# Kernel tuning notes

Measured on AMD Instinct MI355X. Metric: run time of the kernel, lower is better.

## Reference

```python
import jax, jax.numpy as jnp
import numpy as np

NEG_SLOPE = 0.2
EPS = 1e-6


def setup_inputs() -> dict:
    key = jax.random.key(0)
    k1, k2 = jax.random.split(key)
    B, C, N = 4, 64, 32768
    x = jax.random.normal(k1, (B, C, 3, N), dtype=jnp.float32)
    # VNLinear weight: nn.Linear(in, out, bias=False).weight -> [out, in]
    W = jax.random.normal(k2, (C, C), dtype=jnp.float32) * (1.0 / np.sqrt(C))
    return {"x": x, "W": W}


def reference(x, W):
    # VNLinear: kron(W, eye(3)) conv2d == per-3-vector channel mix
    # d[b,o,v,n] = sum_i W[o,i] * x[b,i,v,n]
    d = jnp.einsum('oi,bivn->bovn', W, x)
    dotprod = jnp.sum(x * d, axis=2, keepdims=True)      # [B,C,1,N]
    d_norm_sq = jnp.sum(d * d, axis=2, keepdims=True)    # [B,C,1,N]
    neg = x - (1.0 - NEG_SLOPE) * (dotprod / (d_norm_sq + EPS)) * d
    return jnp.where(dotprod >= 0, x, neg)
```

## Files before the change

kernel.cpp:

```cpp
#include <hip/hip_runtime.h>

#define NEG_SLOPE 0.2f
#define EPS 1e-6f


#define C_CH 64
#define V_DIM 3
#define N_FULL 32768
#define NT 32
#define THREADS 256
#define TPB 4

typedef __attribute__((ext_vector_type(8))) short bf16x8;
typedef __attribute__((ext_vector_type(4))) float f32x4;

__device__ __forceinline__ ushort f2bf(float f) {
    union { float f; unsigned u; } v; v.f = f;
    unsigned r = v.u + 0x7FFFu + ((v.u >> 16) & 1u);
    return (ushort)(r >> 16);
}
__device__ __forceinline__ float bf2f(ushort s) {
    union { unsigned u; float f; } v; v.u = ((unsigned)s) << 16; return v.f;
}
__device__ __forceinline__ unsigned pack_hl(float x) {
    union { float f; unsigned u; } a; a.f = x;
    unsigned t0 = a.u + 0x8000u;
    union { unsigned u; float f; } hb; hb.u = t0 & 0xffff0000u;
    union { float f; unsigned u; } rb; rb.f = x - hb.f;
    return __builtin_amdgcn_perm(t0, rb.u, 0x07060302u);
}

__device__ __forceinline__ int swz(int row) { return ((row >> 3) & 1) << 4; }

__global__ __launch_bounds__(THREADS, 3)
void vn_pipe(const float* __restrict__ x,
             const float* __restrict__ Wf,
             float* __restrict__ out) {
    __shared__ unsigned xs[2][V_DIM * C_CH][NT];

    const int t     = threadIdx.x;
    const int tile0 = blockIdx.x * TPB;
    const int b     = tile0 >> 10;
    const float* xbase = x   + (size_t)b * (C_CH * V_DIM * N_FULL);
    float*       obase = out + (size_t)b * (C_CH * V_DIM * N_FULL);

    const int lane = t & 63;
    const int w    = t >> 6;
    const int wo   = w >> 1;
    const int wn   = w & 1;
    const int l4   = lane & 15;
    const int hi   = lane >> 4;

    float4 xr[6];
    {
        const float* xb = xbase + ((tile0 & 1023) << 5);
        #pragma unroll
        for (int it = 0; it < 6; ++it) {
            int idx = t + it * THREADS;
            xr[it] = *(const float4*)(xb + (size_t)(idx >> 3) * N_FULL + ((idx & 7) << 2));
        }
    }

    bf16x8 Ah[2][2], Al[2][2];
    #pragma unroll
    for (int m = 0; m < 2; ++m)
        #pragma unroll
        for (int kh = 0; kh < 2; ++kh) {
            const float* wp = Wf + (size_t)(wo * 32 + m * 16 + l4) * C_CH + kh * 32 + hi * 8;
            float4 wa = *(const float4*)wp;
            float4 wb = *(const float4*)(wp + 4);
            float wf[8] = {wa.x, wa.y, wa.z, wa.w, wb.x, wb.y, wb.z, wb.w};
            bf16x8 h, l;
            #pragma unroll
            for (int j = 0; j < 8; ++j) {
                ushort hb = f2bf(wf[j]);
                h[j] = (short)hb;
                l[j] = (short)f2bf(wf[j] - bf2f(hb));
            }
            Ah[m][kh] = h; Al[m][kh] = l;
        }

    bf16x8 Aid0, Aid1;
    {
        const int j1 = l4 & 7;
        const bool h0 = (hi == (l4 >> 3));
        const bool h1 = (hi == 2 + (l4 >> 3));
        #pragma unroll
        for (int j = 0; j < 8; ++j) {
            Aid0[j] = (short)((h0 && j == j1) ? 0x3F80 : 0);
            Aid1[j] = (short)((h1 && j == j1) ? 0x3F80 : 0);
        }
    }

    #pragma unroll
    for (int it = 0; it < 6; ++it) {
        int idx = t + it * THREADS;
        int r   = idx >> 3;
        int c4  = (idx & 7) << 2;
        int i   = (r * 171) >> 9;
        int v   = r - 3 * i;
        int rowp = v * 64 + i;
        unsigned p[4] = {pack_hl(xr[it].x), pack_hl(xr[it].y),
                         pack_hl(xr[it].z), pack_hl(xr[it].w)};
        *(uint4*)&xs[0][rowp][c4 ^ swz(rowp)] = *(const uint4*)p;
    }
    __syncthreads();

    const int acol = (wn * 16 + l4) ^ ((hi & 1) << 4);
    const int n    = wn * 16 + l4;

    #pragma unroll
    for (int tt = 0; tt < TPB; ++tt) {
        const int cur = tt & 1;
        const int n0c = ((tile0 + tt) & 1023) << 5;

        if (tt + 1 < TPB) {
            const float* xb = xbase + (((tile0 + tt + 1) & 1023) << 5);
            #pragma unroll
            for (int it = 0; it < 6; ++it) {
                int idx = t + it * THREADS;
                xr[it] = *(const float4*)(xb + (size_t)(idx >> 3) * N_FULL + ((idx & 7) << 2));
            }
        }

        f32x4 acc[2][3], accx[2][3];
        #pragma unroll
        for (int m = 0; m < 2; ++m)
            #pragma unroll
            for (int v = 0; v < 3; ++v) {
                acc[m][v]  = (f32x4){0.f, 0.f, 0.f, 0.f};
                accx[m][v] = (f32x4){0.f, 0.f, 0.f, 0.f};
            }

        #pragma unroll
        for (int v = 0; v < 3; ++v) {
            #pragma unroll
            for (int kh = 0; kh < 2; ++kh) {
                const int rowb = v * 64 + kh * 32 + hi * 8;
                unsigned p[8];
                #pragma unroll
                for (int j = 0; j < 8; ++j)
                    p[j] = xs[cur][rowb + j][acol];
                union { bf16x8 v8; unsigned d[4]; } BH, BL;
                #pragma unroll
                for (int q = 0; q < 4; ++q) {
                    BH.d[q] = __builtin_amdgcn_perm(p[2 * q + 1], p[2 * q], 0x07060302u);
                    BL.d[q] = __builtin_amdgcn_perm(p[2 * q + 1], p[2 * q], 0x05040100u);
                }
                #pragma unroll
                for (int m = 0; m < 2; ++m) {
                    acc[m][v] = __builtin_amdgcn_mfma_f32_16x16x32_bf16(Ah[m][kh], BH.v8, acc[m][v], 0, 0, 0);
                    acc[m][v] = __builtin_amdgcn_mfma_f32_16x16x32_bf16(Ah[m][kh], BL.v8, acc[m][v], 0, 0, 0);
                    acc[m][v] = __builtin_amdgcn_mfma_f32_16x16x32_bf16(Al[m][kh], BH.v8, acc[m][v], 0, 0, 0);
                }
                if (kh == wo) {
                    accx[0][v] = __builtin_amdgcn_mfma_f32_16x16x32_bf16(Aid0, BH.v8, accx[0][v], 0, 0, 0);
                    accx[0][v] = __builtin_amdgcn_mfma_f32_16x16x32_bf16(Aid0, BL.v8, accx[0][v], 0, 0, 0);
                    accx[1][v] = __builtin_amdgcn_mfma_f32_16x16x32_bf16(Aid1, BH.v8, accx[1][v], 0, 0, 0);
                    accx[1][v] = __builtin_amdgcn_mfma_f32_16x16x32_bf16(Aid1, BL.v8, accx[1][v], 0, 0, 0);
                }
            }
        }

        float* ob = obase + n0c + n;
        #pragma unroll
        for (int m = 0; m < 2; ++m) {
            #pragma unroll
            for (int rr = 0; rr < 4; ++rr) {
                const int o = wo * 32 + m * 16 + hi * 4 + rr;
                float xv[3], dv[3];
                #pragma unroll
                for (int v = 0; v < 3; ++v) {
                    xv[v] = accx[m][v][rr];
                    dv[v] = acc[m][v][rr];
                }
                float dot  = xv[0] * dv[0] + xv[1] * dv[1] + xv[2] * dv[2];
                float dnsq = dv[0] * dv[0] + dv[1] * dv[1] + dv[2] * dv[2];
                float f = (1.0f - NEG_SLOPE) * dot * __builtin_amdgcn_rcpf(dnsq + EPS);
                f = (dot >= 0.f) ? 0.f : f;
                float o0 = fmaf(-f, dv[0], xv[0]);
                float o1 = fmaf(-f, dv[1], xv[1]);
                float o2 = fmaf(-f, dv[2], xv[2]);
                float* op = ob + (size_t)o * (V_DIM * N_FULL);
                op[0 * N_FULL] = o0;
                op[1 * N_FULL] = o1;
                op[2 * N_FULL] = o2;
            }
        }

        if (tt + 1 < TPB) {
            #pragma unroll
            for (int it = 0; it < 6; ++it) {
                int idx = t + it * THREADS;
                int r   = idx >> 3;
                int c4  = (idx & 7) << 2;
                int i   = (r * 171) >> 9;
                int v   = r - 3 * i;
                int rowp = v * 64 + i;
                unsigned p[4] = {pack_hl(xr[it].x), pack_hl(xr[it].y),
                                 pack_hl(xr[it].z), pack_hl(xr[it].w)};
                *(uint4*)&xs[cur ^ 1][rowp][c4 ^ swz(rowp)] = *(const uint4*)p;
            }
        }
        __syncthreads();
    }
}

extern "C" void kernel_launch(void* const* d_in, const int* in_sizes, int n_in,
                              void* d_out, int out_size, void* d_ws, size_t ws_size,
                              hipStream_t stream) {
    const float* x = (const float*)d_in[0];
    const float* W = (const float*)d_in[1];
    float* out = (float*)d_out;

    const int B = 4;
    const int blocks = B * (N_FULL / NT) / TPB;
    vn_pipe<<<blocks, THREADS, 0, stream>>>(x, W, out);
}
```

Measured before the change: 37.74 us.

## Stage x tiles into LDS with direct global-to-LDS loads, split bf16 on read

The kernel now uses `__builtin_amdgcn_global_load_lds` to copy raw fp32 x tiles straight into a swizzled LDS buffer. This replaces the old path of loading into registers, packing hi/lo bf16 and writing to LDS. The hi/lo bf16 split now happens after each LDS read, with a truncated hi part and a subtracted remainder. The goal is to cut register pressure and staging VALU work, and to let the prefetch of the next tile overlap fully with the MFMAs. In exchange, the split is redone by every wave that reads the same data, and the code relies on the async loads being properly waited on before the barrier.

```diff
diff --git a/kernel.cpp b/kernel.cpp
--- a/kernel.cpp
+++ b/kernel.cpp
@@ -22,21 +22,18 @@
 __device__ __forceinline__ float bf2f(ushort s) {
     union { unsigned u; float f; } v; v.u = ((unsigned)s) << 16; return v.f;
 }
-__device__ __forceinline__ unsigned pack_hl(float x) {
-    union { float f; unsigned u; } a; a.f = x;
-    unsigned t0 = a.u + 0x8000u;
-    union { unsigned u; float f; } hb; hb.u = t0 & 0xffff0000u;
-    union { float f; unsigned u; } rb; rb.f = x - hb.f;
-    return __builtin_amdgcn_perm(t0, rb.u, 0x07060302u);
+__device__ __forceinline__ unsigned f2u(float f) {
+    union { float f; unsigned u; } v; v.f = f; return v.u;
+}
+__device__ __forceinline__ float u2f(unsigned u) {
+    union { unsigned u; float f; } v; v.u = u; return v.f;
 }
 
-__device__ __forceinline__ int swz(int row) { return ((row >> 3) & 1) << 4; }
-
 __global__ __launch_bounds__(THREADS, 3)
-void vn_pipe(const float* __restrict__ x,
-             const float* __restrict__ Wf,
-             float* __restrict__ out) {
-    __shared__ unsigned xs[2][V_DIM * C_CH][NT];
+void vn_dma_pipe(const float* __restrict__ x,
+                 const float* __restrict__ Wf,
+                 float* __restrict__ out) {
+    __shared__ float xs[2][V_DIM * C_CH * NT];
 
     const int t     = threadIdx.x;
     const int tile0 = blockIdx.x * TPB;
@@ -51,15 +48,9 @@
     const int l4   = lane & 15;
     const int hi   = lane >> 4;
 
-    float4 xr[6];
-    {
-        const float* xb = xbase + ((tile0 & 1023) << 5);
-        #pragma unroll
-        for (int it = 0; it < 6; ++it) {
-            int idx = t + it * THREADS;
-            xr[it] = *(const float4*)(xb + (size_t)(idx >> 3) * N_FULL + ((idx & 7) << 2));
-        }
-    }
+    const int slot_r[6] = { (t + 0*THREADS) >> 3, (t + 1*THREADS) >> 3,
+                            (t + 2*THREADS) >> 3, (t + 3*THREADS) >> 3,
+                            (t + 4*THREADS) >> 3, (t + 5*THREADS) >> 3 };
 
     bf16x8 Ah[2][2], Al[2][2];
     #pragma unroll
@@ -92,18 +83,24 @@
         }
     }
 
-    #pragma unroll
-    for (int it = 0; it < 6; ++it) {
-        int idx = t + it * THREADS;
-        int r   = idx >> 3;
-        int c4  = (idx & 7) << 2;
-        int i   = (r * 171) >> 9;
-        int v   = r - 3 * i;
-        int rowp = v * 64 + i;
-        unsigned p[4] = {pack_hl(xr[it].x), pack_hl(xr[it].y),
-                         pack_hl(xr[it].z), pack_hl(xr[it].w)};
-        *(uint4*)&xs[0][rowp][c4 ^ swz(rowp)] = *(const uint4*)p;
-    }
+    auto stage = [&](int tile, int bf) {
+        const float* xb = xbase + ((tile & 1023) << 5);
+        #pragma unroll
+        for (int it = 0; it < 6; ++it) {
+            int slot = t + it * THREADS;
+            int r    = slot_r[it];
+            int c    = slot & 7;
+            int i    = (r * 171) >> 9;
+            int cs   = c ^ (((i >> 3) & 1) << 2);
+            const float* g = xb + (size_t)r * N_FULL + (cs << 2);
+            void* l = (char*)&xs[bf][0] + (size_t)slot * 16;
+            __builtin_amdgcn_global_load_lds(
+                (const __attribute__((address_space(1))) unsigned*)g,
+                (__attribute__((address_space(3))) unsigned*)l, 16, 0, 0);
+        }
+    };
+
+    stage(tile0, 0);
     __syncthreads();
 
     const int acol = (wn * 16 + l4) ^ ((hi & 1) << 4);
@@ -114,14 +111,7 @@
         const int cur = tt & 1;
         const int n0c = ((tile0 + tt) & 1023) << 5;
 
-        if (tt + 1 < TPB) {
-            const float* xb = xbase + (((tile0 + tt + 1) & 1023) << 5);
-            #pragma unroll
-            for (int it = 0; it < 6; ++it) {
-                int idx = t + it * THREADS;
-                xr[it] = *(const float4*)(xb + (size_t)(idx >> 3) * N_FULL + ((idx & 7) << 2));
-            }
-        }
+        if (tt + 1 < TPB) stage(tile0 + tt + 1, cur ^ 1);
 
         f32x4 acc[2][3], accx[2][3];
         #pragma unroll
@@ -136,16 +126,20 @@
         for (int v = 0; v < 3; ++v) {
             #pragma unroll
             for (int kh = 0; kh < 2; ++kh) {
-                const int rowb = v * 64 + kh * 32 + hi * 8;
-                unsigned p[8];
+                const int ib = kh * 32 + hi * 8;
+                float f[8];
                 #pragma unroll
                 for (int j = 0; j < 8; ++j)
-                    p[j] = xs[cur][rowb + j][acol];
+                    f[j] = xs[cur][(3 * (ib + j) + v) * NT + acol];
                 union { bf16x8 v8; unsigned d[4]; } BH, BL;
+                unsigned rl[8];
+                #pragma unroll
+                for (int j = 0; j < 8; ++j)
+                    rl[j] = f2u(f[j] - u2f(f2u(f[j]) & 0xffff0000u));
                 #pragma unroll
                 for (int q = 0; q < 4; ++q) {
-                    BH.d[q] = __builtin_amdgcn_perm(p[2 * q + 1], p[2 * q], 0x07060302u);
-                    BL.d[q] = __builtin_amdgcn_perm(p[2 * q + 1], p[2 * q], 0x05040100u);
+                    BH.d[q] = __builtin_amdgcn_perm(f2u(f[2 * q + 1]), f2u(f[2 * q]), 0x07060302u);
+                    BL.d[q] = __builtin_amdgcn_perm(rl[2 * q + 1], rl[2 * q], 0x07060302u);
                 }
                 #pragma unroll
                 for (int m = 0; m < 2; ++m) {
@@ -188,20 +182,6 @@
             }
         }
 
-        if (tt + 1 < TPB) {
-            #pragma unroll
-            for (int it = 0; it < 6; ++it) {
-                int idx = t + it * THREADS;
-                int r   = idx >> 3;
-                int c4  = (idx & 7) << 2;
-                int i   = (r * 171) >> 9;
-                int v   = r - 3 * i;
-                int rowp = v * 64 + i;
-                unsigned p[4] = {pack_hl(xr[it].x), pack_hl(xr[it].y),
-                                 pack_hl(xr[it].z), pack_hl(xr[it].w)};
-                *(uint4*)&xs[cur ^ 1][rowp][c4 ^ swz(rowp)] = *(const uint4*)p;
-            }
-        }
         __syncthreads();
     }
 }
@@ -215,5 +195,5 @@
 
     const int B = 4;
     const int blocks = B * (N_FULL / NT) / TPB;
-    vn_pipe<<<blocks, THREADS, 0, stream>>>(x, W, out);
+    vn_dma_pipe<<<blocks, THREADS, 0, stream>>>(x, W, out);
 }
```

Result: slower. 39.93 us (+5.8%).
